# Optimization experiments

Measured on AMD Instinct MI355X. Metric: run time of the kernel, lower is better.

Reference implementation:

```python
import jax, jax.numpy as jnp
import numpy as np

B, T, I, H, O = 256, 512, 512, 512, 1


def setup_inputs() -> dict:
    key = jax.random.key(0)
    ks = jax.random.split(key, 9)
    xavier = lambda k, shape: jax.random.uniform(
        k, shape, jnp.float32,
        -jnp.sqrt(6.0 / (shape[0] + shape[1])), jnp.sqrt(6.0 / (shape[0] + shape[1])))
    return {
        "x":   jax.random.normal(ks[0], (B, T, I), jnp.float32),
        "Wg":  xavier(ks[1], (I + H, 2 * H)),
        "bg":  jnp.zeros((2 * H,), jnp.float32),
        "Wh":  xavier(ks[2], (I + H, H)),
        "bh":  jnp.zeros((H,), jnp.float32),
        "Wo1": xavier(ks[3], (H, H // 2)),
        "bo1": jnp.zeros((H // 2,), jnp.float32),
        "Wo2": xavier(ks[4], (H // 2, O)),
        "bo2": jnp.zeros((O,), jnp.float32),
    }


def reference(x, Wg, bg, Wh, bh, Wo1, bo1, Wo2, bo2):
    # x: [B, T, I]; GRU-style recurrence with fused gate matmul per step.
    Bsz = x.shape[0]
    Hd = Wh.shape[1]

    def step(h, xt):
        xh = jnp.concatenate([xt, h], axis=-1)              # [B, I+H]
        gates = xh @ Wg + bg                                 # [B, 2H]
        update = jax.nn.sigmoid(gates[:, :Hd])
        reset = jax.nn.sigmoid(gates[:, Hd:])
        cand = jnp.tanh(jnp.concatenate([xt, reset * h], axis=-1) @ Wh + bh)
        h_new = (1.0 - update) * h + update * cand
        y = jax.nn.relu(h_new @ Wo1 + bo1) @ Wo2 + bo2       # [B, O]
        return h_new, y

    h0 = jnp.zeros((Bsz, Hd), x.dtype)
    h_final, ys = jax.lax.scan(step, h0, jnp.swapaxes(x, 0, 1))  # ys: [T, B, O]
    return jnp.swapaxes(ys, 0, 1), h_final
```

## Files before the change

### kernel.cpp

```cpp
#include <hip/hip_runtime.h>
#include <hip/hip_bf16.h>
#include <stdint.h>

typedef float f32x4 __attribute__((ext_vector_type(4)));
typedef short bf16x8 __attribute__((ext_vector_type(8)));
typedef int   i32x4  __attribute__((ext_vector_type(4)));

#define DEVINL static __device__ __forceinline__

constexpr int BATCH = 256, SEQ = 512, IDIM = 512, HDIM = 512;
constexpr int NG = 8, WC = 32, RPG = 32, CPW = 16;

constexpr int WGS_OFF = 0;
constexpr int WHS_OFF = 65536;
constexpr int WO1_OFF = 98304;
constexpr int XPOSE_OFF = 114688;
constexpr int SMEM_BYTES = XPOSE_OFF + 2 * 640;

constexpr size_t WS_ZERO = 4096;
constexpr size_t HBF_OFF  = 8192;
constexpr size_t RHBF_OFF = HBF_OFF + 262144;
constexpr size_t WS_NEEDED = RHBF_OFF + 262144;

DEVINL short f2bf(float f) {
  uint32_t u = __float_as_uint(f);
  u += 0x7FFFu + ((u >> 16) & 1u);
  return (short)(u >> 16);
}
DEVINL int wgs_off(int c, int k) { return WGS_OFF + c * 2048 + ((k * 2) ^ ((c & 7) << 4)); }
DEVINL int whs_off(int c, int k) { return WHS_OFF + c * 2048 + ((k * 2) ^ ((c & 7) << 4)); }
DEVINL int wo1_off(int c, int k) { return WO1_OFF + c * 1024 + ((k * 2) ^ ((c & 7) << 4)); }
DEVINL float sigm(float v) { return 1.f / (1.f + __expf(-v)); }
DEVINL bf16x8 asbf(i32x4 v) { return __builtin_bit_cast(bf16x8, v); }

DEVINL void flag_pub(uint32_t* p, uint32_t v) {
  asm volatile("s_waitcnt vmcnt(0) lgkmcnt(0)\n\tglobal_store_dword %0, %1, off sc1"
               :: "v"(p), "v"(v) : "memory");
}
DEVINL void poll32(const uint32_t* base, uint32_t target) {
  const uint32_t* p = base + (threadIdx.x & 31);
  int iter = 0;
  for (;;) {
    uint32_t v;
    asm volatile("global_load_dword %0, %1, off sc1\n\ts_waitcnt vmcnt(0)"
                 : "=v"(v) : "v"(p) : "memory");
    if (__all((int)(v >= target))) break;
    if (++iter > 20000) break;
    __builtin_amdgcn_s_sleep(1);
  }
  __builtin_amdgcn_sched_barrier(0);
}
DEVINL void publish16x16(char* smem, int xpose, short* dst, int grow, int colbase,
                         int lane, const float* vals) {
  const int q = lane >> 4, lc = lane & 15;
#pragma unroll
  for (int ri = 0; ri < 4; ++ri)
    *(short*)(smem + xpose + (q * 4 + ri) * 40 + lc * 2) = f2bf(vals[ri]);
  asm volatile("s_waitcnt lgkmcnt(0)" ::: "memory");
  __builtin_amdgcn_sched_barrier(0);
  const int rl = lane >> 2, cq = lane & 3;
  unsigned long long d = *(const unsigned long long*)(smem + xpose + rl * 40 + cq * 8);
  short* gp = dst + (size_t)(grow + rl) * HDIM + colbase + cq * 4;
  asm volatile("global_store_dwordx2 %0, %1, off sc1" :: "v"(gp), "v"(d) : "memory");
}
#define GLD16(dst, ptr, imm) \
  asm volatile("global_load_dwordx4 %0, %1, off offset:" imm " sc1" : "=v"(dst) : "v"(ptr))
#define GLD_ALL16(arr, ptr) do { \
  GLD16(arr[0],  ptr, "0");   GLD16(arr[1],  ptr, "64");  \
  GLD16(arr[2],  ptr, "128"); GLD16(arr[3],  ptr, "192"); \
  GLD16(arr[4],  ptr, "256"); GLD16(arr[5],  ptr, "320"); \
  GLD16(arr[6],  ptr, "384"); GLD16(arr[7],  ptr, "448"); \
  GLD16(arr[8],  ptr, "512"); GLD16(arr[9],  ptr, "576"); \
  GLD16(arr[10], ptr, "640"); GLD16(arr[11], ptr, "704"); \
  GLD16(arr[12], ptr, "768"); GLD16(arr[13], ptr, "832"); \
  GLD16(arr[14], ptr, "896"); GLD16(arr[15], ptr, "960"); \
  asm volatile("s_waitcnt vmcnt(0)" ::: "memory"); \
  __builtin_amdgcn_sched_barrier(0); \
} while (0)

#define MFMA(a, b, c) __builtin_amdgcn_mfma_f32_16x16x32_bf16((a), (b), (c), 0, 0, 0)
#define LDB(off) (*(const bf16x8*)(smem + (off)))

__global__ void __launch_bounds__(256, 1) init_ys_kernel(float* out, const float* bo2) {
  int i = blockIdx.x * 256 + threadIdx.x;
  if (i < BATCH * SEQ) out[i] = bo2[0];
}

__global__ void __launch_bounds__(128, 1) gru_persist(
    const float* __restrict__ x,  const float* __restrict__ Wg, const float* __restrict__ bg,
    const float* __restrict__ Wh, const float* __restrict__ bh,
    const float* __restrict__ Wo1,const float* __restrict__ bo1,
    const float* __restrict__ Wo2,const float* __restrict__ bo2,
    float* __restrict__ out, char* __restrict__ ws)
{
  extern __shared__ char smem[];
  const int bid  = blockIdx.x;
  const int gi   = bid & 7;
  const int j    = bid >> 3;
  const int tid  = threadIdx.x;
  const int lane = tid & 63;
  const int mt   = tid >> 6;
  const int rowbase = gi * RPG;
  const int colbase = j * CPW;

  short* hbf  = (short*)(ws + HBF_OFF);
  short* rhbf = (short*)(ws + RHBF_OFF);
  uint32_t* fA = (uint32_t*)(ws + (size_t)gi * 512);
  uint32_t* fB = (uint32_t*)(ws + (size_t)gi * 512 + 256);
  const uint32_t* fAmine = fA + mt * 32;
  const uint32_t* fBmine = fB + mt * 32;
  uint32_t* myA = fA + (mt * 32 + j);
  uint32_t* myB = fB + (mt * 32 + j);

  for (int it = 0; it < 256; ++it) {
    int cc = tid & 31;
    int k = (tid >> 5) + it * 4;
    int cg = (cc < 16) ? (colbase + cc) : (512 + colbase + (cc - 16));
    *(short*)(smem + wgs_off(cc, k)) = f2bf(Wg[(size_t)k * 1024 + cg]);
  }
  for (int it = 0; it < 128; ++it) {
    int cc = tid & 15;
    int k = (tid >> 4) + it * 8;
    *(short*)(smem + whs_off(cc, k)) = f2bf(Wh[(size_t)k * 512 + colbase + cc]);
  }
  for (int it = 0; it < 64; ++it) {
    int cc = tid & 15;
    int k = (tid >> 4) + it * 8;
    *(short*)(smem + wo1_off(cc, k)) = (cc < 8) ? f2bf(Wo1[(size_t)k * 256 + j * 8 + cc]) : (short)0;
  }

  const int lc = lane & 15;
  const float bgu  = bg[colbase + lc];
  const float bgr  = bg[512 + colbase + lc];
  const float bhc  = bh[colbase + lc];
  const float bo1c = (lc < 8) ? bo1[j * 8 + lc] : 0.f;
  const float wo2c = (lc < 8) ? Wo2[j * 8 + lc] : 0.f;
  __syncthreads();

  const int arow  = mt * 16 + lc;
  const int kl    = (lane >> 4) * 8;
  const int xpose = XPOSE_OFF + mt * 640;
  const int grow  = rowbase + mt * 16;

  const char* hfrag  = (const char*)(hbf  + (size_t)(rowbase + arow) * HDIM + kl);
  const char* rhfrag = (const char*)(rhbf + (size_t)(rowbase + arow) * HDIM + kl);

  float hreg[4] = {0.f, 0.f, 0.f, 0.f};
  for (int t = 0; t < SEQ; ++t) {
    bf16x8 xa[16];
    {
      const float* xrow = x + ((size_t)(rowbase + arow) * SEQ + t) * IDIM + kl;
#pragma unroll
      for (int ks = 0; ks < 16; ++ks) {
        float4 a = *(const float4*)(xrow + ks * 32);
        float4 b = *(const float4*)(xrow + ks * 32 + 4);
        bf16x8 v;
        v[0] = f2bf(a.x); v[1] = f2bf(a.y); v[2] = f2bf(a.z); v[3] = f2bf(a.w);
        v[4] = f2bf(b.x); v[5] = f2bf(b.y); v[6] = f2bf(b.z); v[7] = f2bf(b.w);
        xa[ks] = v;
      }
    }
    f32x4 gu0 = {0,0,0,0}, gu1 = {0,0,0,0}, gr0 = {0,0,0,0}, gr1 = {0,0,0,0};
#pragma unroll
    for (int ks = 0; ks < 16; ks += 2) {
      gu0 = MFMA(xa[ks],   LDB(wgs_off(lc, ks * 32 + kl)),            gu0);
      gu1 = MFMA(xa[ks+1], LDB(wgs_off(lc, (ks + 1) * 32 + kl)),      gu1);
      gr0 = MFMA(xa[ks],   LDB(wgs_off(16 + lc, ks * 32 + kl)),       gr0);
      gr1 = MFMA(xa[ks+1], LDB(wgs_off(16 + lc, (ks + 1) * 32 + kl)), gr1);
    }
    i32x4 ha[16];
    if (t) {
      poll32(fBmine, (uint32_t)t);
      GLD_ALL16(ha, hfrag);
#pragma unroll
      for (int ks = 0; ks < 16; ks += 2) {
        gu0 = MFMA(asbf(ha[ks]),   LDB(wgs_off(lc, 512 + ks * 32 + kl)),            gu0);
        gu1 = MFMA(asbf(ha[ks+1]), LDB(wgs_off(lc, 512 + (ks + 1) * 32 + kl)),      gu1);
        gr0 = MFMA(asbf(ha[ks]),   LDB(wgs_off(16 + lc, 512 + ks * 32 + kl)),       gr0);
        gr1 = MFMA(asbf(ha[ks+1]), LDB(wgs_off(16 + lc, 512 + (ks + 1) * 32 + kl)), gr1);
      }
    }
    f32x4 gu = gu0 + gu1, gr = gr0 + gr1;
    float uv[4], rhv[4];
#pragma unroll
    for (int ri = 0; ri < 4; ++ri) {
      uv[ri]  = sigm(gu[ri] + bgu);
      rhv[ri] = sigm(gr[ri] + bgr) * hreg[ri];
    }
    if (t) {
      publish16x16(smem, xpose, rhbf, grow, colbase, lane, rhv);
      flag_pub(myA, (uint32_t)(t + 1));
    }
    f32x4 hd0 = {0,0,0,0}, hd1 = {0,0,0,0};
    if (t) {
#pragma unroll
      for (int ks = 0; ks < 16; ks += 2) {
        hd0 = MFMA(asbf(ha[ks]),   LDB(wo1_off(lc, ks * 32 + kl)),       hd0);
        hd1 = MFMA(asbf(ha[ks+1]), LDB(wo1_off(lc, (ks + 1) * 32 + kl)), hd1);
      }
    }
    f32x4 cx0 = {0,0,0,0}, cx1 = {0,0,0,0};
#pragma unroll
    for (int ks = 0; ks < 16; ks += 2) {
      cx0 = MFMA(xa[ks],   LDB(whs_off(lc, ks * 32 + kl)),       cx0);
      cx1 = MFMA(xa[ks+1], LDB(whs_off(lc, (ks + 1) * 32 + kl)), cx1);
    }
    f32x4 ch0 = {0,0,0,0}, ch1 = {0,0,0,0};
    if (t) {
      poll32(fAmine, (uint32_t)(t + 1));
      i32x4 ra[16];
      GLD_ALL16(ra, rhfrag);
#pragma unroll
      for (int ks = 0; ks < 16; ks += 2) {
        ch0 = MFMA(asbf(ra[ks]),   LDB(whs_off(lc, 512 + ks * 32 + kl)),       ch0);
        ch1 = MFMA(asbf(ra[ks+1]), LDB(whs_off(lc, 512 + (ks + 1) * 32 + kl)), ch1);
      }
    }
    f32x4 cc = cx0 + cx1 + ch0 + ch1;
    float hnv[4];
#pragma unroll
    for (int ri = 0; ri < 4; ++ri) {
      float cand = tanhf(cc[ri] + bhc);
      float hnew = hreg[ri] + uv[ri] * (cand - hreg[ri]);
      hreg[ri] = hnew; hnv[ri] = hnew;
      if (t == SEQ - 1) {
        int row = mt * 16 + (lane >> 4) * 4 + ri;
        out[(size_t)(BATCH * SEQ) + (size_t)(rowbase + row) * HDIM + colbase + lc] = hnew;
      }
    }
    publish16x16(smem, xpose, hbf, grow, colbase, lane, hnv);
    flag_pub(myB, (uint32_t)(t + 1));
    if (t) {
      f32x4 d = hd0 + hd1;
#pragma unroll
      for (int ri = 0; ri < 4; ++ri) {
        float z = fmaxf(d[ri] + bo1c, 0.f) * wo2c;
        z += __shfl_xor(z, 1); z += __shfl_xor(z, 2);
        z += __shfl_xor(z, 4); z += __shfl_xor(z, 8);
        if (lc == 0) {
          int row = rowbase + mt * 16 + (lane >> 4) * 4 + ri;
          unsafeAtomicAdd(&out[(size_t)row * SEQ + (t - 1)], z);
        }
      }
    }
  }
  poll32(fBmine, (uint32_t)SEQ);
  i32x4 ha[16];
  GLD_ALL16(ha, hfrag);
  f32x4 hd0 = {0,0,0,0}, hd1 = {0,0,0,0};
#pragma unroll
  for (int ks = 0; ks < 16; ks += 2) {
    hd0 = MFMA(asbf(ha[ks]),   LDB(wo1_off(lc, ks * 32 + kl)),       hd0);
    hd1 = MFMA(asbf(ha[ks+1]), LDB(wo1_off(lc, (ks + 1) * 32 + kl)), hd1);
  }
  f32x4 d = hd0 + hd1;
#pragma unroll
  for (int ri = 0; ri < 4; ++ri) {
    float z = fmaxf(d[ri] + bo1c, 0.f) * wo2c;
    z += __shfl_xor(z, 1); z += __shfl_xor(z, 2);
    z += __shfl_xor(z, 4); z += __shfl_xor(z, 8);
    if (lc == 0) {
      int row = rowbase + mt * 16 + (lane >> 4) * 4 + ri;
      unsafeAtomicAdd(&out[(size_t)row * SEQ + (SEQ - 1)], z);
    }
  }
}

extern "C" void kernel_launch(void* const* d_in, const int* in_sizes, int n_in,
                              void* d_out, int out_size, void* d_ws, size_t ws_size,
                              hipStream_t stream) {
  const float* x   = (const float*)d_in[0];
  const float* Wg  = (const float*)d_in[1];
  const float* bg  = (const float*)d_in[2];
  const float* Wh  = (const float*)d_in[3];
  const float* bh  = (const float*)d_in[4];
  const float* Wo1 = (const float*)d_in[5];
  const float* bo1 = (const float*)d_in[6];
  const float* Wo2 = (const float*)d_in[7];
  const float* bo2 = (const float*)d_in[8];
  float* out = (float*)d_out;
  char*  ws  = (char*)d_ws;
  if (ws_size < WS_NEEDED) return;

  hipMemsetAsync(ws, 0, WS_ZERO, stream);
  init_ys_kernel<<<dim3(512), dim3(256), 0, stream>>>(out, bo2);

  (void)hipFuncSetAttribute((const void*)gru_persist,
                            hipFuncAttributeMaxDynamicSharedMemorySize, SMEM_BYTES);

  gru_persist<<<dim3(NG * WC), dim3(128), SMEM_BYTES, stream>>>(
      x, Wg, bg, Wh, bh, Wo1, bo1, Wo2, bo2, out, ws);
}
```

Baseline: 4.272 ms.

## Use single wave per block handling both 16-row tiles, sharing B fragments

Each block now runs one 64-thread wave that computes both 16-row M tiles, so each weight fragment read from LDS feeds two MFMAs instead of being read by two separate waves. Flags are reduced to one per block, the h/rh publish writes a 32x16 tile with dwordx4 stores, and the x conversion uses packed v_cvt_pk_bf16_f32. This trades wave-level parallelism and latency hiding within a CU for fewer LDS reads, fewer flags to poll and lower sync overhead. Register pressure roughly doubles for the x and h fragments.

```diff
diff --git a/kernel.cpp b/kernel.cpp
--- a/kernel.cpp
+++ b/kernel.cpp
@@ -5,6 +5,7 @@
 typedef float f32x4 __attribute__((ext_vector_type(4)));
 typedef short bf16x8 __attribute__((ext_vector_type(8)));
 typedef int   i32x4  __attribute__((ext_vector_type(4)));
+typedef unsigned int u32x4 __attribute__((ext_vector_type(4)));
 
 #define DEVINL static __device__ __forceinline__
 
@@ -15,7 +16,7 @@
 constexpr int WHS_OFF = 65536;
 constexpr int WO1_OFF = 98304;
 constexpr int XPOSE_OFF = 114688;
-constexpr int SMEM_BYTES = XPOSE_OFF + 2 * 640;
+constexpr int SMEM_BYTES = XPOSE_OFF + 32 * 48;
 
 constexpr size_t WS_ZERO = 4096;
 constexpr size_t HBF_OFF  = 8192;
@@ -26,6 +27,11 @@
   uint32_t u = __float_as_uint(f);
   u += 0x7FFFu + ((u >> 16) & 1u);
   return (short)(u >> 16);
+}
+DEVINL uint32_t cvtpk(float lo, float hi) {
+  uint32_t r;
+  asm("v_cvt_pk_bf16_f32 %0, %1, %2" : "=v"(r) : "v"(lo), "v"(hi));
+  return r;
 }
 DEVINL int wgs_off(int c, int k) { return WGS_OFF + c * 2048 + ((k * 2) ^ ((c & 7) << 4)); }
 DEVINL int whs_off(int c, int k) { return WHS_OFF + c * 2048 + ((k * 2) ^ ((c & 7) << 4)); }
@@ -50,30 +56,34 @@
   }
   __builtin_amdgcn_sched_barrier(0);
 }
-DEVINL void publish16x16(char* smem, int xpose, short* dst, int grow, int colbase,
-                         int lane, const float* vals) {
+DEVINL void publish32x16(char* smem, short* dst, int rowbase, int colbase,
+                         int lane, const float* v0, const float* v1) {
   const int q = lane >> 4, lc = lane & 15;
 #pragma unroll
-  for (int ri = 0; ri < 4; ++ri)
-    *(short*)(smem + xpose + (q * 4 + ri) * 40 + lc * 2) = f2bf(vals[ri]);
+  for (int ri = 0; ri < 4; ++ri) {
+    *(short*)(smem + XPOSE_OFF + (q * 4 + ri) * 48 + lc * 2)      = f2bf(v0[ri]);
+    *(short*)(smem + XPOSE_OFF + (16 + q * 4 + ri) * 48 + lc * 2) = f2bf(v1[ri]);
+  }
   asm volatile("s_waitcnt lgkmcnt(0)" ::: "memory");
   __builtin_amdgcn_sched_barrier(0);
-  const int rl = lane >> 2, cq = lane & 3;
-  unsigned long long d = *(const unsigned long long*)(smem + xpose + rl * 40 + cq * 8);
-  short* gp = dst + (size_t)(grow + rl) * HDIM + colbase + cq * 4;
-  asm volatile("global_store_dwordx2 %0, %1, off sc1" :: "v"(gp), "v"(d) : "memory");
-}
-#define GLD16(dst, ptr, imm) \
+  const int rl = lane >> 1, half = lane & 1;
+  i32x4 d = *(const i32x4*)(smem + XPOSE_OFF + rl * 48 + half * 16);
+  short* gp = dst + (size_t)(rowbase + rl) * HDIM + colbase + half * 8;
+  asm volatile("global_store_dwordx4 %0, %1, off sc1" :: "v"(gp), "v"(d) : "memory");
+}
+#define GLD16NF(dst, ptr, imm) \
   asm volatile("global_load_dwordx4 %0, %1, off offset:" imm " sc1" : "=v"(dst) : "v"(ptr))
-#define GLD_ALL16(arr, ptr) do { \
-  GLD16(arr[0],  ptr, "0");   GLD16(arr[1],  ptr, "64");  \
-  GLD16(arr[2],  ptr, "128"); GLD16(arr[3],  ptr, "192"); \
-  GLD16(arr[4],  ptr, "256"); GLD16(arr[5],  ptr, "320"); \
-  GLD16(arr[6],  ptr, "384"); GLD16(arr[7],  ptr, "448"); \
-  GLD16(arr[8],  ptr, "512"); GLD16(arr[9],  ptr, "576"); \
-  GLD16(arr[10], ptr, "640"); GLD16(arr[11], ptr, "704"); \
-  GLD16(arr[12], ptr, "768"); GLD16(arr[13], ptr, "832"); \
-  GLD16(arr[14], ptr, "896"); GLD16(arr[15], ptr, "960"); \
+#define GLD_BATCH16(arr, ptr) do { \
+  GLD16NF(arr[0],  ptr, "0");   GLD16NF(arr[1],  ptr, "64");  \
+  GLD16NF(arr[2],  ptr, "128"); GLD16NF(arr[3],  ptr, "192"); \
+  GLD16NF(arr[4],  ptr, "256"); GLD16NF(arr[5],  ptr, "320"); \
+  GLD16NF(arr[6],  ptr, "384"); GLD16NF(arr[7],  ptr, "448"); \
+  GLD16NF(arr[8],  ptr, "512"); GLD16NF(arr[9],  ptr, "576"); \
+  GLD16NF(arr[10], ptr, "640"); GLD16NF(arr[11], ptr, "704"); \
+  GLD16NF(arr[12], ptr, "768"); GLD16NF(arr[13], ptr, "832"); \
+  GLD16NF(arr[14], ptr, "896"); GLD16NF(arr[15], ptr, "960"); \
+} while (0)
+#define GLD_FENCE() do { \
   asm volatile("s_waitcnt vmcnt(0)" ::: "memory"); \
   __builtin_amdgcn_sched_barrier(0); \
 } while (0)
@@ -86,7 +96,7 @@
   if (i < BATCH * SEQ) out[i] = bo2[0];
 }
 
-__global__ void __launch_bounds__(128, 1) gru_persist(
+__global__ void __launch_bounds__(64, 1) gru_persist(
     const float* __restrict__ x,  const float* __restrict__ Wg, const float* __restrict__ bg,
     const float* __restrict__ Wh, const float* __restrict__ bh,
     const float* __restrict__ Wo1,const float* __restrict__ bo1,
@@ -99,7 +109,6 @@
   const int j    = bid >> 3;
   const int tid  = threadIdx.x;
   const int lane = tid & 63;
-  const int mt   = tid >> 6;
   const int rowbase = gi * RPG;
   const int colbase = j * CPW;
 
@@ -107,29 +116,28 @@
   short* rhbf = (short*)(ws + RHBF_OFF);
   uint32_t* fA = (uint32_t*)(ws + (size_t)gi * 512);
   uint32_t* fB = (uint32_t*)(ws + (size_t)gi * 512 + 256);
-  const uint32_t* fAmine = fA + mt * 32;
-  const uint32_t* fBmine = fB + mt * 32;
-  uint32_t* myA = fA + (mt * 32 + j);
-  uint32_t* myB = fB + (mt * 32 + j);
-
-  for (int it = 0; it < 256; ++it) {
-    int cc = tid & 31;
-    int k = (tid >> 5) + it * 4;
+  uint32_t* myA = fA + j;
+  uint32_t* myB = fB + j;
+
+  for (int it = 0; it < 512; ++it) {
+    int idx = it * 64 + tid;
+    int cc = idx & 31, k = idx >> 5;
     int cg = (cc < 16) ? (colbase + cc) : (512 + colbase + (cc - 16));
     *(short*)(smem + wgs_off(cc, k)) = f2bf(Wg[(size_t)k * 1024 + cg]);
   }
+  for (int it = 0; it < 256; ++it) {
+    int idx = it * 64 + tid;
+    int cc = idx & 15, k = idx >> 4;
+    *(short*)(smem + whs_off(cc, k)) = f2bf(Wh[(size_t)k * 512 + colbase + cc]);
+  }
   for (int it = 0; it < 128; ++it) {
-    int cc = tid & 15;
-    int k = (tid >> 4) + it * 8;
-    *(short*)(smem + whs_off(cc, k)) = f2bf(Wh[(size_t)k * 512 + colbase + cc]);
-  }
-  for (int it = 0; it < 64; ++it) {
-    int cc = tid & 15;
-    int k = (tid >> 4) + it * 8;
+    int idx = it * 64 + tid;
+    int cc = idx & 15, k = idx >> 4;
     *(short*)(smem + wo1_off(cc, k)) = (cc < 8) ? f2bf(Wo1[(size_t)k * 256 + j * 8 + cc]) : (short)0;
   }
 
   const int lc = lane & 15;
+  const int kl = (lane >> 4) * 8;
   const float bgu  = bg[colbase + lc];
   const float bgr  = bg[512 + colbase + lc];
   const float bhc  = bh[colbase + lc];
@@ -137,131 +145,157 @@
   const float wo2c = (lc < 8) ? Wo2[j * 8 + lc] : 0.f;
   __syncthreads();
 
-  const int arow  = mt * 16 + lc;
-  const int kl    = (lane >> 4) * 8;
-  const int xpose = XPOSE_OFF + mt * 640;
-  const int grow  = rowbase + mt * 16;
-
-  const char* hfrag  = (const char*)(hbf  + (size_t)(rowbase + arow) * HDIM + kl);
-  const char* rhfrag = (const char*)(rhbf + (size_t)(rowbase + arow) * HDIM + kl);
-
-  float hreg[4] = {0.f, 0.f, 0.f, 0.f};
+  const char* hfrag0  = (const char*)(hbf  + (size_t)(rowbase + lc) * HDIM + kl);
+  const char* hfrag1  = hfrag0 + (size_t)16 * HDIM * 2;
+  const char* rhfrag0 = (const char*)(rhbf + (size_t)(rowbase + lc) * HDIM + kl);
+  const char* rhfrag1 = rhfrag0 + (size_t)16 * HDIM * 2;
+
+  float hreg0[4] = {0,0,0,0}, hreg1[4] = {0,0,0,0};
+
   for (int t = 0; t < SEQ; ++t) {
-    bf16x8 xa[16];
+    bf16x8 xa0[16], xa1[16];
     {
-      const float* xrow = x + ((size_t)(rowbase + arow) * SEQ + t) * IDIM + kl;
-#pragma unroll
-      for (int ks = 0; ks < 16; ++ks) {
-        float4 a = *(const float4*)(xrow + ks * 32);
-        float4 b = *(const float4*)(xrow + ks * 32 + 4);
-        bf16x8 v;
-        v[0] = f2bf(a.x); v[1] = f2bf(a.y); v[2] = f2bf(a.z); v[3] = f2bf(a.w);
-        v[4] = f2bf(b.x); v[5] = f2bf(b.y); v[6] = f2bf(b.z); v[7] = f2bf(b.w);
-        xa[ks] = v;
+      const float* xr0 = x + ((size_t)(rowbase + lc) * SEQ + t) * IDIM + kl;
+      const float* xr1 = xr0 + (size_t)16 * SEQ * IDIM;
+#pragma unroll
+      for (int ks = 0; ks < 16; ++ks) {
+        float4 a = *(const float4*)(xr0 + ks * 32);
+        float4 b = *(const float4*)(xr0 + ks * 32 + 4);
+        u32x4 v = {cvtpk(a.x, a.y), cvtpk(a.z, a.w), cvtpk(b.x, b.y), cvtpk(b.z, b.w)};
+        xa0[ks] = __builtin_bit_cast(bf16x8, v);
+      }
+#pragma unroll
+      for (int ks = 0; ks < 16; ++ks) {
+        float4 a = *(const float4*)(xr1 + ks * 32);
+        float4 b = *(const float4*)(xr1 + ks * 32 + 4);
+        u32x4 v = {cvtpk(a.x, a.y), cvtpk(a.z, a.w), cvtpk(b.x, b.y), cvtpk(b.z, b.w)};
+        xa1[ks] = __builtin_bit_cast(bf16x8, v);
       }
     }
     f32x4 gu0 = {0,0,0,0}, gu1 = {0,0,0,0}, gr0 = {0,0,0,0}, gr1 = {0,0,0,0};
 #pragma unroll
-    for (int ks = 0; ks < 16; ks += 2) {
-      gu0 = MFMA(xa[ks],   LDB(wgs_off(lc, ks * 32 + kl)),            gu0);
-      gu1 = MFMA(xa[ks+1], LDB(wgs_off(lc, (ks + 1) * 32 + kl)),      gu1);
-      gr0 = MFMA(xa[ks],   LDB(wgs_off(16 + lc, ks * 32 + kl)),       gr0);
-      gr1 = MFMA(xa[ks+1], LDB(wgs_off(16 + lc, (ks + 1) * 32 + kl)), gr1);
-    }
-    i32x4 ha[16];
-    if (t) {
-      poll32(fBmine, (uint32_t)t);
-      GLD_ALL16(ha, hfrag);
-#pragma unroll
-      for (int ks = 0; ks < 16; ks += 2) {
-        gu0 = MFMA(asbf(ha[ks]),   LDB(wgs_off(lc, 512 + ks * 32 + kl)),            gu0);
-        gu1 = MFMA(asbf(ha[ks+1]), LDB(wgs_off(lc, 512 + (ks + 1) * 32 + kl)),      gu1);
-        gr0 = MFMA(asbf(ha[ks]),   LDB(wgs_off(16 + lc, 512 + ks * 32 + kl)),       gr0);
-        gr1 = MFMA(asbf(ha[ks+1]), LDB(wgs_off(16 + lc, 512 + (ks + 1) * 32 + kl)), gr1);
-      }
-    }
-    f32x4 gu = gu0 + gu1, gr = gr0 + gr1;
-    float uv[4], rhv[4];
+    for (int ks = 0; ks < 16; ++ks) {
+      bf16x8 bu = LDB(wgs_off(lc, ks * 32 + kl));
+      bf16x8 br = LDB(wgs_off(16 + lc, ks * 32 + kl));
+      gu0 = MFMA(xa0[ks], bu, gu0);
+      gu1 = MFMA(xa1[ks], bu, gu1);
+      gr0 = MFMA(xa0[ks], br, gr0);
+      gr1 = MFMA(xa1[ks], br, gr1);
+    }
+    i32x4 ha0[16], ha1[16];
+    if (t) {
+      poll32(fB, (uint32_t)t);
+      GLD_BATCH16(ha0, hfrag0);
+      GLD_BATCH16(ha1, hfrag1);
+      GLD_FENCE();
+#pragma unroll
+      for (int ks = 0; ks < 16; ++ks) {
+        bf16x8 bu = LDB(wgs_off(lc, 512 + ks * 32 + kl));
+        bf16x8 br = LDB(wgs_off(16 + lc, 512 + ks * 32 + kl));
+        gu0 = MFMA(asbf(ha0[ks]), bu, gu0);
+        gu1 = MFMA(asbf(ha1[ks]), bu, gu1);
+        gr0 = MFMA(asbf(ha0[ks]), br, gr0);
+        gr1 = MFMA(asbf(ha1[ks]), br, gr1);
+      }
+    }
+    float uv0[4], uv1[4], rhv0[4], rhv1[4];
 #pragma unroll
     for (int ri = 0; ri < 4; ++ri) {
-      uv[ri]  = sigm(gu[ri] + bgu);
-      rhv[ri] = sigm(gr[ri] + bgr) * hreg[ri];
-    }
-    if (t) {
-      publish16x16(smem, xpose, rhbf, grow, colbase, lane, rhv);
+      uv0[ri]  = sigm(gu0[ri] + bgu);
+      uv1[ri]  = sigm(gu1[ri] + bgu);
+      rhv0[ri] = sigm(gr0[ri] + bgr) * hreg0[ri];
+      rhv1[ri] = sigm(gr1[ri] + bgr) * hreg1[ri];
+    }
+    if (t) {
+      publish32x16(smem, rhbf, rowbase, colbase, lane, rhv0, rhv1);
       flag_pub(myA, (uint32_t)(t + 1));
     }
     f32x4 hd0 = {0,0,0,0}, hd1 = {0,0,0,0};
     if (t) {
 #pragma unroll
-      for (int ks = 0; ks < 16; ks += 2) {
-        hd0 = MFMA(asbf(ha[ks]),   LDB(wo1_off(lc, ks * 32 + kl)),       hd0);
-        hd1 = MFMA(asbf(ha[ks+1]), LDB(wo1_off(lc, (ks + 1) * 32 + kl)), hd1);
+      for (int ks = 0; ks < 16; ++ks) {
+        bf16x8 bo = LDB(wo1_off(lc, ks * 32 + kl));
+        hd0 = MFMA(asbf(ha0[ks]), bo, hd0);
+        hd1 = MFMA(asbf(ha1[ks]), bo, hd1);
       }
     }
     f32x4 cx0 = {0,0,0,0}, cx1 = {0,0,0,0};
 #pragma unroll
-    for (int ks = 0; ks < 16; ks += 2) {
-      cx0 = MFMA(xa[ks],   LDB(whs_off(lc, ks * 32 + kl)),       cx0);
-      cx1 = MFMA(xa[ks+1], LDB(whs_off(lc, (ks + 1) * 32 + kl)), cx1);
-    }
-    f32x4 ch0 = {0,0,0,0}, ch1 = {0,0,0,0};
-    if (t) {
-      poll32(fAmine, (uint32_t)(t + 1));
-      i32x4 ra[16];
-      GLD_ALL16(ra, rhfrag);
-#pragma unroll
-      for (int ks = 0; ks < 16; ks += 2) {
-        ch0 = MFMA(asbf(ra[ks]),   LDB(whs_off(lc, 512 + ks * 32 + kl)),       ch0);
-        ch1 = MFMA(asbf(ra[ks+1]), LDB(whs_off(lc, 512 + (ks + 1) * 32 + kl)), ch1);
-      }
-    }
-    f32x4 cc = cx0 + cx1 + ch0 + ch1;
-    float hnv[4];
+    for (int ks = 0; ks < 16; ++ks) {
+      bf16x8 bc = LDB(whs_off(lc, ks * 32 + kl));
+      cx0 = MFMA(xa0[ks], bc, cx0);
+      cx1 = MFMA(xa1[ks], bc, cx1);
+    }
+    if (t) {
+      i32x4 ra0[16], ra1[16];
+      poll32(fA, (uint32_t)(t + 1));
+      GLD_BATCH16(ra0, rhfrag0);
+      GLD_BATCH16(ra1, rhfrag1);
+      GLD_FENCE();
+#pragma unroll
+      for (int ks = 0; ks < 16; ++ks) {
+        bf16x8 bc = LDB(whs_off(lc, 512 + ks * 32 + kl));
+        cx0 = MFMA(asbf(ra0[ks]), bc, cx0);
+        cx1 = MFMA(asbf(ra1[ks]), bc, cx1);
+      }
+    }
+    float hnv0[4], hnv1[4];
 #pragma unroll
     for (int ri = 0; ri < 4; ++ri) {
-      float cand = tanhf(cc[ri] + bhc);
-      float hnew = hreg[ri] + uv[ri] * (cand - hreg[ri]);
-      hreg[ri] = hnew; hnv[ri] = hnew;
+      float c0 = tanhf(cx0[ri] + bhc);
+      float c1 = tanhf(cx1[ri] + bhc);
+      float h0 = hreg0[ri] + uv0[ri] * (c0 - hreg0[ri]);
+      float h1 = hreg1[ri] + uv1[ri] * (c1 - hreg1[ri]);
+      hreg0[ri] = h0; hreg1[ri] = h1; hnv0[ri] = h0; hnv1[ri] = h1;
       if (t == SEQ - 1) {
-        int row = mt * 16 + (lane >> 4) * 4 + ri;
-        out[(size_t)(BATCH * SEQ) + (size_t)(rowbase + row) * HDIM + colbase + lc] = hnew;
-      }
-    }
-    publish16x16(smem, xpose, hbf, grow, colbase, lane, hnv);
+        int r0 = (lane >> 4) * 4 + ri;
+        out[(size_t)(BATCH * SEQ) + (size_t)(rowbase + r0) * HDIM + colbase + lc] = h0;
+        out[(size_t)(BATCH * SEQ) + (size_t)(rowbase + 16 + r0) * HDIM + colbase + lc] = h1;
+      }
+    }
+    publish32x16(smem, hbf, rowbase, colbase, lane, hnv0, hnv1);
     flag_pub(myB, (uint32_t)(t + 1));
     if (t) {
-      f32x4 d = hd0 + hd1;
 #pragma unroll
       for (int ri = 0; ri < 4; ++ri) {
-        float z = fmaxf(d[ri] + bo1c, 0.f) * wo2c;
-        z += __shfl_xor(z, 1); z += __shfl_xor(z, 2);
-        z += __shfl_xor(z, 4); z += __shfl_xor(z, 8);
+        float z0 = fmaxf(hd0[ri] + bo1c, 0.f) * wo2c;
+        float z1 = fmaxf(hd1[ri] + bo1c, 0.f) * wo2c;
+        z0 += __shfl_xor(z0, 1); z0 += __shfl_xor(z0, 2);
+        z0 += __shfl_xor(z0, 4); z0 += __shfl_xor(z0, 8);
+        z1 += __shfl_xor(z1, 1); z1 += __shfl_xor(z1, 2);
+        z1 += __shfl_xor(z1, 4); z1 += __shfl_xor(z1, 8);
         if (lc == 0) {
-          int row = rowbase + mt * 16 + (lane >> 4) * 4 + ri;
-          unsafeAtomicAdd(&out[(size_t)row * SEQ + (t - 1)], z);
+          int r0 = rowbase + (lane >> 4) * 4 + ri;
+          unsafeAtomicAdd(&out[(size_t)r0 * SEQ + (t - 1)], z0);
+          unsafeAtomicAdd(&out[(size_t)(r0 + 16) * SEQ + (t - 1)], z1);
         }
       }
     }
   }
-  poll32(fBmine, (uint32_t)SEQ);
-  i32x4 ha[16];
-  GLD_ALL16(ha, hfrag);
+  poll32(fB, (uint32_t)SEQ);
+  i32x4 ha0[16], ha1[16];
+  GLD_BATCH16(ha0, hfrag0);
+  GLD_BATCH16(ha1, hfrag1);
+  GLD_FENCE();
   f32x4 hd0 = {0,0,0,0}, hd1 = {0,0,0,0};
 #pragma unroll
-  for (int ks = 0; ks < 16; ks += 2) {
-    hd0 = MFMA(asbf(ha[ks]),   LDB(wo1_off(lc, ks * 32 + kl)),       hd0);
-    hd1 = MFMA(asbf(ha[ks+1]), LDB(wo1_off(lc, (ks + 1) * 32 + kl)), hd1);
-  }
-  f32x4 d = hd0 + hd1;
+  for (int ks = 0; ks < 16; ++ks) {
+    bf16x8 bo = LDB(wo1_off(lc, ks * 32 + kl));
+    hd0 = MFMA(asbf(ha0[ks]), bo, hd0);
+    hd1 = MFMA(asbf(ha1[ks]), bo, hd1);
+  }
 #pragma unroll
   for (int ri = 0; ri < 4; ++ri) {
-    float z = fmaxf(d[ri] + bo1c, 0.f) * wo2c;
-    z += __shfl_xor(z, 1); z += __shfl_xor(z, 2);
-    z += __shfl_xor(z, 4); z += __shfl_xor(z, 8);
+    float z0 = fmaxf(hd0[ri] + bo1c, 0.f) * wo2c;
+    float z1 = fmaxf(hd1[ri] + bo1c, 0.f) * wo2c;
+    z0 += __shfl_xor(z0, 1); z0 += __shfl_xor(z0, 2);
+    z0 += __shfl_xor(z0, 4); z0 += __shfl_xor(z0, 8);
+    z1 += __shfl_xor(z1, 1); z1 += __shfl_xor(z1, 2);
+    z1 += __shfl_xor(z1, 4); z1 += __shfl_xor(z1, 8);
     if (lc == 0) {
-      int row = rowbase + mt * 16 + (lane >> 4) * 4 + ri;
-      unsafeAtomicAdd(&out[(size_t)row * SEQ + (SEQ - 1)], z);
+      int r0 = rowbase + (lane >> 4) * 4 + ri;
+      unsafeAtomicAdd(&out[(size_t)r0 * SEQ + (SEQ - 1)], z0);
+      unsafeAtomicAdd(&out[(size_t)(r0 + 16) * SEQ + (SEQ - 1)], z1);
     }
   }
 }
@@ -288,6 +322,6 @@
   (void)hipFuncSetAttribute((const void*)gru_persist,
                             hipFuncAttributeMaxDynamicSharedMemorySize, SMEM_BYTES);
 
-  gru_persist<<<dim3(NG * WC), dim3(128), SMEM_BYTES, stream>>>(
+  gru_persist<<<dim3(NG * WC), dim3(64), SMEM_BYTES, stream>>>(
       x, Wg, bg, Wh, bh, Wo1, bo1, Wo2, bo2, out, ws);
 }
```

After: 13.34 ms. 3.12x slower.

## Prefetch next-step x gates before publishing flags and use packed bf16 conversion

Applied to the files above, without the earlier changes.

Moves the x-load, bf16 conversion and x-part gate MFMAs for step t+1 to just after publishing h for step t but before its flag store. That work now overlaps the cross-block flag latency instead of sitting at the start of the next step. The reset-flag publish is also delayed until after the candidate x MFMAs, giving the rh stores time to land while other work runs. Scalar rounding is replaced with the hardware v_cvt_pk_bf16_f32 instruction. The catch is that the flag store's waitcnt now also waits on the x global loads, which can delay the handoff of h to other blocks.

```diff
diff --git a/kernel.cpp b/kernel.cpp
--- a/kernel.cpp
+++ b/kernel.cpp
@@ -5,6 +5,7 @@
 typedef float f32x4 __attribute__((ext_vector_type(4)));
 typedef short bf16x8 __attribute__((ext_vector_type(8)));
 typedef int   i32x4  __attribute__((ext_vector_type(4)));
+typedef unsigned int u32x4 __attribute__((ext_vector_type(4)));
 
 #define DEVINL static __device__ __forceinline__
 
@@ -26,6 +27,11 @@
   uint32_t u = __float_as_uint(f);
   u += 0x7FFFu + ((u >> 16) & 1u);
   return (short)(u >> 16);
+}
+DEVINL uint32_t cvtpk(float lo, float hi) {
+  uint32_t r;
+  asm("v_cvt_pk_bf16_f32 %0, %1, %2" : "=v"(r) : "v"(lo), "v"(hi));
+  return r;
 }
 DEVINL int wgs_off(int c, int k) { return WGS_OFF + c * 2048 + ((k * 2) ^ ((c & 7) << 4)); }
 DEVINL int whs_off(int c, int k) { return WHS_OFF + c * 2048 + ((k * 2) ^ ((c & 7) << 4)); }
@@ -80,6 +86,29 @@
 
 #define MFMA(a, b, c) __builtin_amdgcn_mfma_f32_16x16x32_bf16((a), (b), (c), 0, 0, 0)
 #define LDB(off) (*(const bf16x8*)(smem + (off)))
+
+#define LOADCVT_X(tt) do { \
+  const float* xr_ = x + ((size_t)(rowbase + arow) * SEQ + (size_t)(tt)) * IDIM + kl; \
+  _Pragma("unroll") \
+  for (int ks = 0; ks < 16; ++ks) { \
+    float4 a_ = *(const float4*)(xr_ + ks * 32); \
+    float4 b_ = *(const float4*)(xr_ + ks * 32 + 4); \
+    u32x4 v_ = {cvtpk(a_.x, a_.y), cvtpk(a_.z, a_.w), \
+                cvtpk(b_.x, b_.y), cvtpk(b_.z, b_.w)}; \
+    xa[ks] = __builtin_bit_cast(bf16x8, v_); \
+  } \
+} while (0)
+#define GATES_X() do { \
+  gu0 = (f32x4){0,0,0,0}; gu1 = (f32x4){0,0,0,0}; \
+  gr0 = (f32x4){0,0,0,0}; gr1 = (f32x4){0,0,0,0}; \
+  _Pragma("unroll") \
+  for (int ks = 0; ks < 16; ks += 2) { \
+    gu0 = MFMA(xa[ks],   LDB(wgs_off(lc, ks * 32 + kl)),            gu0); \
+    gu1 = MFMA(xa[ks+1], LDB(wgs_off(lc, (ks + 1) * 32 + kl)),      gu1); \
+    gr0 = MFMA(xa[ks],   LDB(wgs_off(16 + lc, ks * 32 + kl)),       gr0); \
+    gr1 = MFMA(xa[ks+1], LDB(wgs_off(16 + lc, (ks + 1) * 32 + kl)), gr1); \
+  } \
+} while (0)
 
 __global__ void __launch_bounds__(256, 1) init_ys_kernel(float* out, const float* bo2) {
   int i = blockIdx.x * 256 + threadIdx.x;
@@ -145,29 +174,14 @@
   const char* hfrag  = (const char*)(hbf  + (size_t)(rowbase + arow) * HDIM + kl);
   const char* rhfrag = (const char*)(rhbf + (size_t)(rowbase + arow) * HDIM + kl);
 
+  bf16x8 xa[16];
+  f32x4 gu0, gu1, gr0, gr1;
+
+  LOADCVT_X(0);
+  GATES_X();
+
   float hreg[4] = {0.f, 0.f, 0.f, 0.f};
   for (int t = 0; t < SEQ; ++t) {
-    bf16x8 xa[16];
-    {
-      const float* xrow = x + ((size_t)(rowbase + arow) * SEQ + t) * IDIM + kl;
-#pragma unroll
-      for (int ks = 0; ks < 16; ++ks) {
-        float4 a = *(const float4*)(xrow + ks * 32);
-        float4 b = *(const float4*)(xrow + ks * 32 + 4);
-        bf16x8 v;
-        v[0] = f2bf(a.x); v[1] = f2bf(a.y); v[2] = f2bf(a.z); v[3] = f2bf(a.w);
-        v[4] = f2bf(b.x); v[5] = f2bf(b.y); v[6] = f2bf(b.z); v[7] = f2bf(b.w);
-        xa[ks] = v;
-      }
-    }
-    f32x4 gu0 = {0,0,0,0}, gu1 = {0,0,0,0}, gr0 = {0,0,0,0}, gr1 = {0,0,0,0};
-#pragma unroll
-    for (int ks = 0; ks < 16; ks += 2) {
-      gu0 = MFMA(xa[ks],   LDB(wgs_off(lc, ks * 32 + kl)),            gu0);
-      gu1 = MFMA(xa[ks+1], LDB(wgs_off(lc, (ks + 1) * 32 + kl)),      gu1);
-      gr0 = MFMA(xa[ks],   LDB(wgs_off(16 + lc, ks * 32 + kl)),       gr0);
-      gr1 = MFMA(xa[ks+1], LDB(wgs_off(16 + lc, (ks + 1) * 32 + kl)), gr1);
-    }
     i32x4 ha[16];
     if (t) {
       poll32(fBmine, (uint32_t)t);
@@ -187,10 +201,7 @@
       uv[ri]  = sigm(gu[ri] + bgu);
       rhv[ri] = sigm(gr[ri] + bgr) * hreg[ri];
     }
-    if (t) {
-      publish16x16(smem, xpose, rhbf, grow, colbase, lane, rhv);
-      flag_pub(myA, (uint32_t)(t + 1));
-    }
+    if (t) publish16x16(smem, xpose, rhbf, grow, colbase, lane, rhv);
     f32x4 hd0 = {0,0,0,0}, hd1 = {0,0,0,0};
     if (t) {
 #pragma unroll
@@ -205,6 +216,7 @@
       cx0 = MFMA(xa[ks],   LDB(whs_off(lc, ks * 32 + kl)),       cx0);
       cx1 = MFMA(xa[ks+1], LDB(whs_off(lc, (ks + 1) * 32 + kl)), cx1);
     }
+    if (t) flag_pub(myA, (uint32_t)(t + 1));
     f32x4 ch0 = {0,0,0,0}, ch1 = {0,0,0,0};
     if (t) {
       poll32(fAmine, (uint32_t)(t + 1));
@@ -229,6 +241,10 @@
       }
     }
     publish16x16(smem, xpose, hbf, grow, colbase, lane, hnv);
+    if (t < SEQ - 1) {
+      LOADCVT_X(t + 1);
+      GATES_X();
+    }
     flag_pub(myB, (uint32_t)(t + 1));
     if (t) {
       f32x4 d = hd0 + hd1;
```

Result: slower. 8.294 ms (+94.2%).

## Offload output head to a dedicated wave with double-buffered hidden state

Applied to the files above, without the earlier changes.

Adds a third wave per block that polls the published hidden state and computes the Wo1/Wo2 output head and atomic adds, taking that work off the two recurrence waves. The hidden state buffer is double-buffered so the head wave can read step t-1 while the recurrence writes step t, with a new progress flag that the recurrence checks before overwriting. The reset-gate MFMAs are reordered ahead of the update-gate MFMAs so r*h can be published earlier on the critical path. The x conversion now uses packed v_cvt_pk_bf16_f32. The risks are extra polling traffic and more register pressure from 192 threads per block.

```diff
diff --git a/kernel.cpp b/kernel.cpp
--- a/kernel.cpp
+++ b/kernel.cpp
@@ -5,6 +5,7 @@
 typedef float f32x4 __attribute__((ext_vector_type(4)));
 typedef short bf16x8 __attribute__((ext_vector_type(8)));
 typedef int   i32x4  __attribute__((ext_vector_type(4)));
+typedef unsigned int u32x4 __attribute__((ext_vector_type(4)));
 
 #define DEVINL static __device__ __forceinline__
 
@@ -17,15 +18,21 @@
 constexpr int XPOSE_OFF = 114688;
 constexpr int SMEM_BYTES = XPOSE_OFF + 2 * 640;
 
-constexpr size_t WS_ZERO = 4096;
-constexpr size_t HBF_OFF  = 8192;
-constexpr size_t RHBF_OFF = HBF_OFF + 262144;
+constexpr size_t WS_ZERO  = 8192;
+constexpr size_t HBF0_OFF = 8192;
+constexpr size_t HBF1_OFF = HBF0_OFF + 262144;
+constexpr size_t RHBF_OFF = HBF1_OFF + 262144;
 constexpr size_t WS_NEEDED = RHBF_OFF + 262144;
 
 DEVINL short f2bf(float f) {
   uint32_t u = __float_as_uint(f);
   u += 0x7FFFu + ((u >> 16) & 1u);
   return (short)(u >> 16);
+}
+DEVINL uint32_t cvtpk(float lo, float hi) {
+  uint32_t r;
+  asm("v_cvt_pk_bf16_f32 %0, %1, %2" : "=v"(r) : "v"(lo), "v"(hi));
+  return r;
 }
 DEVINL int wgs_off(int c, int k) { return WGS_OFF + c * 2048 + ((k * 2) ^ ((c & 7) << 4)); }
 DEVINL int whs_off(int c, int k) { return WHS_OFF + c * 2048 + ((k * 2) ^ ((c & 7) << 4)); }
@@ -36,6 +43,9 @@
 DEVINL void flag_pub(uint32_t* p, uint32_t v) {
   asm volatile("s_waitcnt vmcnt(0) lgkmcnt(0)\n\tglobal_store_dword %0, %1, off sc1"
                :: "v"(p), "v"(v) : "memory");
+}
+DEVINL void flag_raw(uint32_t* p, uint32_t v) {
+  asm volatile("global_store_dword %0, %1, off sc1" :: "v"(p), "v"(v) : "memory");
 }
 DEVINL void poll32(const uint32_t* base, uint32_t target) {
   const uint32_t* p = base + (threadIdx.x & 31);
@@ -46,6 +56,35 @@
                  : "=v"(v) : "v"(p) : "memory");
     if (__all((int)(v >= target))) break;
     if (++iter > 20000) break;
+    __builtin_amdgcn_s_sleep(1);
+  }
+  __builtin_amdgcn_sched_barrier(0);
+}
+DEVINL void pollA_dual(const uint32_t* baseA, const uint32_t* baseH,
+                       uint32_t tA, uint32_t tH) {
+  const int l = threadIdx.x & 63;
+  const uint32_t* p = (l < 32) ? (baseA + l) : (baseH + (l - 32));
+  const uint32_t tgt = (l < 32) ? tA : tH;
+  int iter = 0;
+  for (;;) {
+    uint32_t v;
+    asm volatile("global_load_dword %0, %1, off sc1\n\ts_waitcnt vmcnt(0)"
+                 : "=v"(v) : "v"(p) : "memory");
+    if (__all((int)(v >= tgt))) break;
+    if (++iter > 20000) break;
+    __builtin_amdgcn_s_sleep(1);
+  }
+  __builtin_amdgcn_sched_barrier(0);
+}
+DEVINL void poll64(const uint32_t* base, uint32_t target) {
+  const uint32_t* p = base + (threadIdx.x & 63);
+  int iter = 0;
+  for (;;) {
+    uint32_t v;
+    asm volatile("global_load_dword %0, %1, off sc1\n\ts_waitcnt vmcnt(0)"
+                 : "=v"(v) : "v"(p) : "memory");
+    if (__all((int)(v >= target))) break;
+    if (++iter > 40000) break;
     __builtin_amdgcn_s_sleep(1);
   }
   __builtin_amdgcn_sched_barrier(0);
@@ -81,12 +120,24 @@
 #define MFMA(a, b, c) __builtin_amdgcn_mfma_f32_16x16x32_bf16((a), (b), (c), 0, 0, 0)
 #define LDB(off) (*(const bf16x8*)(smem + (off)))
 
+#define LOADCVT_X(tt) do { \
+  const float* xr_ = x + ((size_t)(rowbase + arow) * SEQ + (size_t)(tt)) * IDIM + kl; \
+  _Pragma("unroll") \
+  for (int ks = 0; ks < 16; ++ks) { \
+    float4 a_ = *(const float4*)(xr_ + ks * 32); \
+    float4 b_ = *(const float4*)(xr_ + ks * 32 + 4); \
+    u32x4 v_ = {cvtpk(a_.x, a_.y), cvtpk(a_.z, a_.w), \
+                cvtpk(b_.x, b_.y), cvtpk(b_.z, b_.w)}; \
+    xa[ks] = __builtin_bit_cast(bf16x8, v_); \
+  } \
+} while (0)
+
 __global__ void __launch_bounds__(256, 1) init_ys_kernel(float* out, const float* bo2) {
   int i = blockIdx.x * 256 + threadIdx.x;
   if (i < BATCH * SEQ) out[i] = bo2[0];
 }
 
-__global__ void __launch_bounds__(128, 1) gru_persist(
+__global__ void __launch_bounds__(192, 1) gru_persist(
     const float* __restrict__ x,  const float* __restrict__ Wg, const float* __restrict__ bg,
     const float* __restrict__ Wh, const float* __restrict__ bh,
     const float* __restrict__ Wo1,const float* __restrict__ bo1,
@@ -99,37 +150,33 @@
   const int j    = bid >> 3;
   const int tid  = threadIdx.x;
   const int lane = tid & 63;
-  const int mt   = tid >> 6;
+  const int wave = tid >> 6;
   const int rowbase = gi * RPG;
   const int colbase = j * CPW;
 
-  short* hbf  = (short*)(ws + HBF_OFF);
+  short* hbf0 = (short*)(ws + HBF0_OFF);
+  short* hbf1 = (short*)(ws + HBF1_OFF);
   short* rhbf = (short*)(ws + RHBF_OFF);
-  uint32_t* fA = (uint32_t*)(ws + (size_t)gi * 512);
-  uint32_t* fB = (uint32_t*)(ws + (size_t)gi * 512 + 256);
-  const uint32_t* fAmine = fA + mt * 32;
-  const uint32_t* fBmine = fB + mt * 32;
-  uint32_t* myA = fA + (mt * 32 + j);
-  uint32_t* myB = fB + (mt * 32 + j);
-
-  for (int it = 0; it < 256; ++it) {
-    int cc = tid & 31;
-    int k = (tid >> 5) + it * 4;
+  uint32_t* fA = (uint32_t*)(ws + (size_t)gi * 1024);
+  uint32_t* fB = (uint32_t*)(ws + (size_t)gi * 1024 + 256);
+  uint32_t* hp = (uint32_t*)(ws + (size_t)gi * 1024 + 512);
+
+  for (int idx = tid; idx < 32 * 1024; idx += 192) {
+    int cc = idx & 31, k = idx >> 5;
     int cg = (cc < 16) ? (colbase + cc) : (512 + colbase + (cc - 16));
     *(short*)(smem + wgs_off(cc, k)) = f2bf(Wg[(size_t)k * 1024 + cg]);
   }
-  for (int it = 0; it < 128; ++it) {
-    int cc = tid & 15;
-    int k = (tid >> 4) + it * 8;
+  for (int idx = tid; idx < 16 * 1024; idx += 192) {
+    int cc = idx & 15, k = idx >> 4;
     *(short*)(smem + whs_off(cc, k)) = f2bf(Wh[(size_t)k * 512 + colbase + cc]);
   }
-  for (int it = 0; it < 64; ++it) {
-    int cc = tid & 15;
-    int k = (tid >> 4) + it * 8;
+  for (int idx = tid; idx < 16 * 512; idx += 192) {
+    int cc = idx & 15, k = idx >> 4;
     *(short*)(smem + wo1_off(cc, k)) = (cc < 8) ? f2bf(Wo1[(size_t)k * 256 + j * 8 + cc]) : (short)0;
   }
 
   const int lc = lane & 15;
+  const int kl = (lane >> 4) * 8;
   const float bgu  = bg[colbase + lc];
   const float bgr  = bg[512 + colbase + lc];
   const float bhc  = bh[colbase + lc];
@@ -137,29 +184,62 @@
   const float wo2c = (lc < 8) ? Wo2[j * 8 + lc] : 0.f;
   __syncthreads();
 
+  if (wave == 2) {
+    const size_t ro0 = (size_t)(rowbase + lc) * HDIM + kl;
+    const size_t ro1 = ro0 + (size_t)16 * HDIM;
+    uint32_t* myhp = hp + j;
+    for (int t = 1; t <= SEQ; ++t) {
+      poll64(fB, (uint32_t)t);
+      const short* hb = ((t - 1) & 1) ? hbf1 : hbf0;
+      i32x4 ha0[16], ha1[16];
+      GLD_ALL16(ha0, (const char*)(hb + ro0));
+      GLD_ALL16(ha1, (const char*)(hb + ro1));
+      flag_raw(myhp, (uint32_t)t);
+      f32x4 hd0 = {0,0,0,0}, hd1 = {0,0,0,0};
+#pragma unroll
+      for (int ks = 0; ks < 16; ks += 2) {
+        hd0 = MFMA(asbf(ha0[ks]),   LDB(wo1_off(lc, ks * 32 + kl)),       hd0);
+        hd0 = MFMA(asbf(ha0[ks+1]), LDB(wo1_off(lc, (ks + 1) * 32 + kl)), hd0);
+        hd1 = MFMA(asbf(ha1[ks]),   LDB(wo1_off(lc, ks * 32 + kl)),       hd1);
+        hd1 = MFMA(asbf(ha1[ks+1]), LDB(wo1_off(lc, (ks + 1) * 32 + kl)), hd1);
+      }
+#pragma unroll
+      for (int ri = 0; ri < 4; ++ri) {
+        float z0 = fmaxf(hd0[ri] + bo1c, 0.f) * wo2c;
+        float z1 = fmaxf(hd1[ri] + bo1c, 0.f) * wo2c;
+        z0 += __shfl_xor(z0, 1); z0 += __shfl_xor(z0, 2);
+        z0 += __shfl_xor(z0, 4); z0 += __shfl_xor(z0, 8);
+        z1 += __shfl_xor(z1, 1); z1 += __shfl_xor(z1, 2);
+        z1 += __shfl_xor(z1, 4); z1 += __shfl_xor(z1, 8);
+        if (lc == 0) {
+          int r0 = rowbase + (lane >> 4) * 4 + ri;
+          unsafeAtomicAdd(&out[(size_t)r0 * SEQ + (t - 1)], z0);
+          unsafeAtomicAdd(&out[(size_t)(r0 + 16) * SEQ + (t - 1)], z1);
+        }
+      }
+    }
+    return;
+  }
+
+  const int mt    = wave;
   const int arow  = mt * 16 + lc;
-  const int kl    = (lane >> 4) * 8;
   const int xpose = XPOSE_OFF + mt * 640;
   const int grow  = rowbase + mt * 16;
-
-  const char* hfrag  = (const char*)(hbf  + (size_t)(rowbase + arow) * HDIM + kl);
-  const char* rhfrag = (const char*)(rhbf + (size_t)(rowbase + arow) * HDIM + kl);
-
+  const uint32_t* fAmine = fA + mt * 32;
+  const uint32_t* fBmine = fB + mt * 32;
+  uint32_t* myA = fA + (mt * 32 + j);
+  uint32_t* myB = fB + (mt * 32 + j);
+
+  const size_t hro = (size_t)(rowbase + arow) * HDIM + kl;
+  const char* hfrag0 = (const char*)(hbf0 + hro);
+  const char* hfrag1 = (const char*)(hbf1 + hro);
+  const char* rhfrag = (const char*)(rhbf + hro);
+
+  bf16x8 xa[16];
   float hreg[4] = {0.f, 0.f, 0.f, 0.f};
+
   for (int t = 0; t < SEQ; ++t) {
-    bf16x8 xa[16];
-    {
-      const float* xrow = x + ((size_t)(rowbase + arow) * SEQ + t) * IDIM + kl;
-#pragma unroll
-      for (int ks = 0; ks < 16; ++ks) {
-        float4 a = *(const float4*)(xrow + ks * 32);
-        float4 b = *(const float4*)(xrow + ks * 32 + 4);
-        bf16x8 v;
-        v[0] = f2bf(a.x); v[1] = f2bf(a.y); v[2] = f2bf(a.z); v[3] = f2bf(a.w);
-        v[4] = f2bf(b.x); v[5] = f2bf(b.y); v[6] = f2bf(b.z); v[7] = f2bf(b.w);
-        xa[ks] = v;
-      }
-    }
+    LOADCVT_X(t);
     f32x4 gu0 = {0,0,0,0}, gu1 = {0,0,0,0}, gr0 = {0,0,0,0}, gr1 = {0,0,0,0};
 #pragma unroll
     for (int ks = 0; ks < 16; ks += 2) {
@@ -171,34 +251,32 @@
     i32x4 ha[16];
     if (t) {
       poll32(fBmine, (uint32_t)t);
-      GLD_ALL16(ha, hfrag);
+      GLD_ALL16(ha, ((t - 1) & 1) ? hfrag1 : hfrag0);
 #pragma unroll
       for (int ks = 0; ks < 16; ks += 2) {
-        gu0 = MFMA(asbf(ha[ks]),   LDB(wgs_off(lc, 512 + ks * 32 + kl)),            gu0);
-        gu1 = MFMA(asbf(ha[ks+1]), LDB(wgs_off(lc, 512 + (ks + 1) * 32 + kl)),      gu1);
         gr0 = MFMA(asbf(ha[ks]),   LDB(wgs_off(16 + lc, 512 + ks * 32 + kl)),       gr0);
         gr1 = MFMA(asbf(ha[ks+1]), LDB(wgs_off(16 + lc, 512 + (ks + 1) * 32 + kl)), gr1);
       }
     }
-    f32x4 gu = gu0 + gu1, gr = gr0 + gr1;
-    float uv[4], rhv[4];
-#pragma unroll
-    for (int ri = 0; ri < 4; ++ri) {
-      uv[ri]  = sigm(gu[ri] + bgu);
-      rhv[ri] = sigm(gr[ri] + bgr) * hreg[ri];
-    }
+    f32x4 gr = gr0 + gr1;
+    float rhv[4];
+#pragma unroll
+    for (int ri = 0; ri < 4; ++ri) rhv[ri] = sigm(gr[ri] + bgr) * hreg[ri];
     if (t) {
       publish16x16(smem, xpose, rhbf, grow, colbase, lane, rhv);
       flag_pub(myA, (uint32_t)(t + 1));
     }
-    f32x4 hd0 = {0,0,0,0}, hd1 = {0,0,0,0};
     if (t) {
 #pragma unroll
       for (int ks = 0; ks < 16; ks += 2) {
-        hd0 = MFMA(asbf(ha[ks]),   LDB(wo1_off(lc, ks * 32 + kl)),       hd0);
-        hd1 = MFMA(asbf(ha[ks+1]), LDB(wo1_off(lc, (ks + 1) * 32 + kl)), hd1);
-      }
-    }
+        gu0 = MFMA(asbf(ha[ks]),   LDB(wgs_off(lc, 512 + ks * 32 + kl)),       gu0);
+        gu1 = MFMA(asbf(ha[ks+1]), LDB(wgs_off(lc, 512 + (ks + 1) * 32 + kl)), gu1);
+      }
+    }
+    f32x4 gu = gu0 + gu1;
+    float uv[4];
+#pragma unroll
+    for (int ri = 0; ri < 4; ++ri) uv[ri] = sigm(gu[ri] + bgu);
     f32x4 cx0 = {0,0,0,0}, cx1 = {0,0,0,0};
 #pragma unroll
     for (int ks = 0; ks < 16; ks += 2) {
@@ -207,7 +285,7 @@
     }
     f32x4 ch0 = {0,0,0,0}, ch1 = {0,0,0,0};
     if (t) {
-      poll32(fAmine, (uint32_t)(t + 1));
+      pollA_dual(fAmine, hp, (uint32_t)(t + 1), (uint32_t)(t - 1));
       i32x4 ra[16];
       GLD_ALL16(ra, rhfrag);
 #pragma unroll
@@ -228,41 +306,8 @@
         out[(size_t)(BATCH * SEQ) + (size_t)(rowbase + row) * HDIM + colbase + lc] = hnew;
       }
     }
-    publish16x16(smem, xpose, hbf, grow, colbase, lane, hnv);
+    publish16x16(smem, xpose, (t & 1) ? hbf1 : hbf0, grow, colbase, lane, hnv);
     flag_pub(myB, (uint32_t)(t + 1));
-    if (t) {
-      f32x4 d = hd0 + hd1;
-#pragma unroll
-      for (int ri = 0; ri < 4; ++ri) {
-        float z = fmaxf(d[ri] + bo1c, 0.f) * wo2c;
-        z += __shfl_xor(z, 1); z += __shfl_xor(z, 2);
-        z += __shfl_xor(z, 4); z += __shfl_xor(z, 8);
-        if (lc == 0) {
-          int row = rowbase + mt * 16 + (lane >> 4) * 4 + ri;
-          unsafeAtomicAdd(&out[(size_t)row * SEQ + (t - 1)], z);
-        }
-      }
-    }
-  }
-  poll32(fBmine, (uint32_t)SEQ);
-  i32x4 ha[16];
-  GLD_ALL16(ha, hfrag);
-  f32x4 hd0 = {0,0,0,0}, hd1 = {0,0,0,0};
-#pragma unroll
-  for (int ks = 0; ks < 16; ks += 2) {
-    hd0 = MFMA(asbf(ha[ks]),   LDB(wo1_off(lc, ks * 32 + kl)),       hd0);
-    hd1 = MFMA(asbf(ha[ks+1]), LDB(wo1_off(lc, (ks + 1) * 32 + kl)), hd1);
-  }
-  f32x4 d = hd0 + hd1;
-#pragma unroll
-  for (int ri = 0; ri < 4; ++ri) {
-    float z = fmaxf(d[ri] + bo1c, 0.f) * wo2c;
-    z += __shfl_xor(z, 1); z += __shfl_xor(z, 2);
-    z += __shfl_xor(z, 4); z += __shfl_xor(z, 8);
-    if (lc == 0) {
-      int row = rowbase + mt * 16 + (lane >> 4) * 4 + ri;
-      unsafeAtomicAdd(&out[(size_t)row * SEQ + (SEQ - 1)], z);
-    }
   }
 }
 
@@ -288,6 +333,6 @@
   (void)hipFuncSetAttribute((const void*)gru_persist,
                             hipFuncAttributeMaxDynamicSharedMemorySize, SMEM_BYTES);
 
-  gru_persist<<<dim3(NG * WC), dim3(128), SMEM_BYTES, stream>>>(
+  gru_persist<<<dim3(NG * WC), dim3(192), SMEM_BYTES, stream>>>(
       x, Wg, bg, Wh, bh, Wo1, bo1, Wo2, bo2, out, ws);
 }
```

Measured after the change: 8.408 ms. 96.8% more time.
